# Kernel tuning notes

Measured on AMD Instinct MI355X. Metric: run time of the kernel, lower is better.

The kernel has to match this reference:

```python
import jax, jax.numpy as jnp
import numpy as np

B, T, H, L, V = 32, 512, 1024, 256, 13  # V = FDIM_JOINT_VOCAB_DECODING


def setup_inputs() -> dict:
    key = jax.random.key(0)
    ks = jax.random.split(key, 16)
    s_in = 1.0 / np.sqrt(V)
    s_h = 1.0 / np.sqrt(H)
    s_l = 1.0 / np.sqrt(L)
    s_hl = 1.0 / np.sqrt(H + L)
    # one-hot-like teacher-forced inputs (first token is all-zero start token)
    labels = jax.random.randint(ks[0], (B, T), 0, V)
    seq_input = jax.nn.one_hot(labels, V, dtype=jnp.float32)
    seq_input = jnp.concatenate([jnp.zeros((B, 1, V), jnp.float32), seq_input[:, :-1]], axis=1)
    lengths = jax.random.randint(ks[1], (B,), T // 2, T + 1).astype(jnp.int32)
    return {
        "seq_input": seq_input,
        "latent_vec": jax.random.normal(ks[2], (B, L), jnp.float32),
        "labels": labels.astype(jnp.int32),
        "lengths": lengths,
        "W_ih": jax.random.uniform(ks[3], (4 * H, V), jnp.float32, -s_h, s_h),
        "W_hh": jax.random.uniform(ks[4], (4 * H, H), jnp.float32, -s_h, s_h),
        "b_ih": jax.random.uniform(ks[5], (4 * H,), jnp.float32, -s_h, s_h),
        "b_hh": jax.random.uniform(ks[6], (4 * H,), jnp.float32, -s_h, s_h),
        "Wz": jax.random.uniform(ks[7], (H, L), jnp.float32, -s_l, s_l),
        "bz": jax.random.uniform(ks[8], (H,), jnp.float32, -s_l, s_l),
        "Wnl": jax.random.uniform(ks[9], (H, H + L), jnp.float32, -s_hl, s_hl),
        "bnl": jax.random.uniform(ks[10], (H,), jnp.float32, -s_hl, s_hl),
        "Wout": jax.random.uniform(ks[11], (V, H), jnp.float32, -s_h, s_h),
        "bout": jax.random.uniform(ks[12], (V,), jnp.float32, -s_h, s_h),
    }


def _forward(seq_input, latent_vec, labels, lengths,
             W_ih, W_hh, b_ih, b_hh, Wz, bz, Wnl, bnl, Wout, bout):
    h0 = jax.nn.relu(latent_vec @ Wz.T + bz)              # [B,H]
    c0 = jnp.zeros_like(h0)

    def step(carry, x_t):
        h, c = carry
        gates = x_t @ W_ih.T + b_ih + h @ W_hh.T + b_hh   # [B,4H]
        i, f, g, o = jnp.split(gates, 4, axis=-1)         # torch LSTMCell gate order
        c = jax.nn.sigmoid(f) * c + jax.nn.sigmoid(i) * jnp.tanh(g)
        h = jax.nn.sigmoid(o) * jnp.tanh(c)
        return (h, c), h

    xs = jnp.swapaxes(seq_input, 0, 1)                    # [T,B,V]
    _, hs = jax.lax.scan(step, (h0, c0), xs)              # [T,B,H]
    hs = jnp.swapaxes(hs, 0, 1)                           # [B,T,H]

    # aggregate: cat(h, z) -> relu(W_nonlinear) -> W
    lat = jnp.broadcast_to(latent_vec[:, None, :], (hs.shape[0], hs.shape[1], latent_vec.shape[-1]))
    feat = jnp.concatenate([hs, lat], axis=-1)            # [B,T,H+L]
    logits = jax.nn.relu(feat @ Wnl.T + bnl) @ Wout.T + bout  # [B,T,V]

    logp = jax.nn.log_softmax(logits, axis=-1)
    nll = -jnp.take_along_axis(logp, labels[..., None].astype(jnp.int32), axis=-1)[..., 0]  # [B,T]
    mask = (jnp.arange(T)[None, :] < lengths[:, None]).astype(nll.dtype)
    batch_loss = jnp.sum(nll * mask, axis=1)              # per-sequence segment sum
    return batch_loss


def reference(seq_input, latent_vec, labels, lengths,
              W_ih, W_hh, b_ih, b_hh, Wz, bz, Wnl, bnl, Wout, bout):
    batch_loss = _forward(seq_input, latent_vec, labels, lengths,
                          W_ih, W_hh, b_ih, b_hh, Wz, bz, Wnl, bnl, Wout, bout)
    return jnp.sum(batch_loss), batch_loss
```

## Files before the change

kernel.cpp:

```cpp
#include <hip/hip_runtime.h>
#include <hip/hip_bf16.h>

#define B_   32
#define T_   512
#define H_   1024
#define L_   256
#define V_   13
#define G4H  4096
#define KHL  1280

typedef float f32x4 __attribute__((ext_vector_type(4)));
typedef short s16x8 __attribute__((ext_vector_type(8)));
typedef unsigned short u16;
typedef unsigned int   u32;
typedef unsigned long long u64;

#define OFF_BF   33619968u
#define OFF_BF2  42008576u
#define OFF_AZ   44630016u
#define OFF_BAR  44646400u
#define OFF_MID  44650496u
#define OFF_GX   OFF_MID
#define OFF_TOK  (OFF_MID + 229376u)

__device__ __forceinline__ u16 f2bf(float f) {
    union { float f; u32 u; } v; v.f = f;
    u32 u = v.u;
    u32 r = (u + 0x7fffu + ((u >> 16) & 1u)) >> 16;
    return (u16)r;
}
__device__ __forceinline__ float bf2f(u16 h) {
    union { u32 u; float f; } v; v.u = ((u32)h) << 16;
    return v.f;
}
__device__ __forceinline__ float sigm_(float x) {
    x = fminf(fmaxf(x, -30.f), 30.f);
    return 1.f / (1.f + __expf(-x));
}
__device__ __forceinline__ float tanh_(float x) {
    x = fminf(fmaxf(x, -15.f), 15.f);
    float e = __expf(2.f * x);
    return (e - 1.f) / (e + 1.f);
}

__device__ __forceinline__ u32 afrag_pos(int bl, int k) {
    return (u32)((k >> 5) * 512 + ((bl | (((k >> 3) & 3) << 4)) << 3) + (k & 7));
}

__global__ __launch_bounds__(256) void k_init_misc(
        const float* __restrict__ latent, const float* __restrict__ Wz,
        const float* __restrict__ bz,
        u16* __restrict__ Ax, u16* __restrict__ Az, int* __restrict__ bar) {
    int gid = blockIdx.x * 256 + threadIdx.x;
    int b = gid >> 10, j = gid & 1023;
    const float* lrow = latent + b * L_;
    const float* wrow = Wz + j * L_;
    float acc = bz[j];
    #pragma unroll 4
    for (int l = 0; l < L_; ++l) acc += lrow[l] * wrow[l];
    Ax[(b >> 4) * 16384 + afrag_pos(b & 15, j)] = f2bf(fmaxf(acc, 0.f));
    if (gid < B_ * L_) {
        int bb = gid >> 8, l = gid & 255;
        Az[(bb >> 4) * 4096 + afrag_pos(bb & 15, l)] = f2bf(latent[gid]);
    }
    if (gid < 1024) bar[gid] = 0;
}

__global__ __launch_bounds__(256) void k_init_gx(
        const float* __restrict__ W_ih, const float* __restrict__ b_ih,
        const float* __restrict__ b_hh, float* __restrict__ Gx) {
    int row = blockIdx.x * 256 + threadIdx.x;
    if (row >= G4H) return;
    int gg = row >> 10, jg = row & 1023;
    float base = b_ih[row] + b_hh[row];
    float* d = Gx + (size_t)jg * 56;
    const float* wr = W_ih + (size_t)row * V_;
    #pragma unroll
    for (int t = 0; t < V_; ++t) d[t * 4 + gg] = base + wr[t];
    d[13 * 4 + gg] = base;
}

__global__ __launch_bounds__(256) void k_init_tok(
        const float* __restrict__ seq, u16* __restrict__ tok) {
    int gid = blockIdx.x * 256 + threadIdx.x;
    int s = gid >> 5, b = gid & 31;
    const float* r = seq + ((size_t)b * T_ + s) * V_;
    int t = 13;
    #pragma unroll
    for (int v = 0; v < V_; ++v) if (r[v] > 0.5f) t = v;
    tok[gid] = (u16)t;
}

__global__ __launch_bounds__(256) void k_init_wfrag(
        const float* __restrict__ W_hh, u16* __restrict__ Bf) {
    int base = blockIdx.x * 256 + threadIdx.x;
    #pragma unroll
    for (int i = 0; i < 8; ++i) {
        int idx = base + i * 524288;
        int jv   = idx & 7;
        int lane = (idx >> 3) & 63;
        int kc   = (idx >> 9) & 31;
        int nt   = idx >> 14;
        int u = lane & 15;
        int row = (u & 3) * H_ + nt * 4 + (u >> 2);
        int k = kc * 32 + (lane >> 4) * 8 + jv;
        Bf[idx] = f2bf(W_hh[row * H_ + k]);
    }
}

__global__ __launch_bounds__(256) void k_init_wfrag2(
        const float* __restrict__ Wnl, u16* __restrict__ Bf2) {
    int idx = blockIdx.x * 256 + threadIdx.x;
    for (; idx < 1310720; idx += 524288) {
        int jv   = idx & 7;
        int lane = (idx >> 3) & 63;
        int q    = idx >> 9;
        int kc   = q % 40;
        int nt2  = q / 40;
        int n = nt2 * 16 + (lane & 15);
        int k = kc * 32 + (lane >> 4) * 8 + jv;
        Bf2[idx] = f2bf(Wnl[n * KHL + k]);
    }
}

__global__ __launch_bounds__(512, 1) void k_recur(
        const u16* __restrict__ tokbuf, const float* __restrict__ Gx,
        const u16* __restrict__ Bf, u16* __restrict__ Ax,
        int* __restrict__ bar) {
    __shared__ uint4 AhV[2048];
    int tid = threadIdx.x;
    int bid = blockIdx.x;
    int mt = bid & 1;
    int p  = bid >> 1;
    int w = tid >> 6, L = tid & 63;
    int nt = p * 8 + w;
    int lm = L & 15, quad = L >> 4;

    s16x8 afr[32];
    {
        const u16* bfp = Bf + (size_t)nt * 16384 + L * 8;
        #pragma unroll
        for (int kc = 0; kc < 32; ++kc)
            afr[kc] = *reinterpret_cast<const s16x8*>(bfp + kc * 512);
    }
    int jg = nt * 4 + quad;
    int b = mt * 16 + lm;
    const float* gxp = Gx + (size_t)jg * 56;
    u32 posu16 = (u32)((nt >> 3) * 512 + ((lm | (((nt >> 1) & 3) << 4)) << 3)
                       + (nt & 1) * 4 + quad);
    int* flags = bar + mt * 512;
    const int* myflag = flags + (w + 8 * (L & 3)) * 16;
    u32* AxD = (u32*)Ax;
    float c = 0.f;

    for (int s = 0; s < T_; ++s) {
        int tok = tokbuf[s * 32 + b];
        float4 gx4 = *reinterpret_cast<const float4*>(gxp + tok * 4);

        for (;;) {
            int v = __hip_atomic_load(myflag, __ATOMIC_RELAXED,
                                      __HIP_MEMORY_SCOPE_AGENT);
            if (__all(v >= s)) break;
            __builtin_amdgcn_s_sleep(1);
        }
        const uint4* srcq = (const uint4*)((const char*)Ax
                             + ((size_t)s * 2 + mt) * 32768);
        #pragma unroll
        for (int i = 0; i < 4; ++i)
            AhV[i * 512 + tid] = srcq[i * 512 + tid];
        __syncthreads();

        f32x4 a0 = {0.f,0.f,0.f,0.f}, a1 = {0.f,0.f,0.f,0.f};
        f32x4 a2 = {0.f,0.f,0.f,0.f}, a3 = {0.f,0.f,0.f,0.f};
        const u16* hp = (const u16*)AhV + L * 8;
        #pragma unroll
        for (int kc = 0; kc < 32; kc += 4) {
            s16x8 h0 = *reinterpret_cast<const s16x8*>(hp + kc * 512);
            s16x8 h1 = *reinterpret_cast<const s16x8*>(hp + (kc + 1) * 512);
            s16x8 h2 = *reinterpret_cast<const s16x8*>(hp + (kc + 2) * 512);
            s16x8 h3 = *reinterpret_cast<const s16x8*>(hp + (kc + 3) * 512);
            a0 = __builtin_amdgcn_mfma_f32_16x16x32_bf16(afr[kc],     h0, a0, 0, 0, 0);
            a1 = __builtin_amdgcn_mfma_f32_16x16x32_bf16(afr[kc + 1], h1, a1, 0, 0, 0);
            a2 = __builtin_amdgcn_mfma_f32_16x16x32_bf16(afr[kc + 2], h2, a2, 0, 0, 0);
            a3 = __builtin_amdgcn_mfma_f32_16x16x32_bf16(afr[kc + 3], h3, a3, 0, 0, 0);
        }
        float gi = a0[0] + a1[0] + a2[0] + a3[0] + gx4.x;
        float gf = a0[1] + a1[1] + a2[1] + a3[1] + gx4.y;
        float gg = a0[2] + a1[2] + a2[2] + a3[2] + gx4.z;
        float go = a0[3] + a1[3] + a2[3] + a3[3] + gx4.w;
        float ig = sigm_(gi), fg = sigm_(gf);
        float gt = tanh_(gg), og = sigm_(go);
        c = fg * c + ig * gt;
        float hv = og * tanh_(c);

        u32 bits = (u32)f2bf(hv);
        u32 other = (u32)(u16)__shfl_xor((int)bits, 16);
        if (!(quad & 1)) {
            u32 word = bits | (other << 16);
            __hip_atomic_store(
                AxD + ((size_t)(s + 1) * 2 + mt) * 8192 + (posu16 >> 1),
                word, __ATOMIC_RELAXED, __HIP_MEMORY_SCOPE_AGENT);
        }
        if (s == T_ - 1) break;
        __syncthreads();
        if (tid == 0)
            __hip_atomic_store(flags + p * 16, s + 1, __ATOMIC_RELAXED,
                               __HIP_MEMORY_SCOPE_AGENT);
    }
}

__global__ __launch_bounds__(256) void k_gemm1(
        const u16* __restrict__ Ax, const u16* __restrict__ Az,
        const u16* __restrict__ Bf2, const float* __restrict__ bnl,
        u16* __restrict__ mid) {
    int tid = threadIdx.x;
    int nb = blockIdx.x;
    int mb = blockIdx.y;
    int w = tid >> 6, L = tid & 63;
    int lm = L & 15, quad = L >> 4;
    int mti0 = mb * 8 + w * 2;
    const u16* a0p = Ax + ((size_t)mti0 + 2) * 16384 + L * 8;
    const u16* a1p = a0p + 16384;
    const u16* az0 = Az + L * 8;
    const u16* az1 = az0 + 4096;
    const u16* bp = Bf2 + (size_t)(nb * 4) * 40 * 512 + L * 8;

    f32x4 acc[2][4];
    #pragma unroll
    for (int a = 0; a < 2; ++a)
        #pragma unroll
        for (int n = 0; n < 4; ++n) acc[a][n] = (f32x4){0.f, 0.f, 0.f, 0.f};

    #pragma unroll 4
    for (int kc = 0; kc < 32; ++kc) {
        s16x8 a0 = *reinterpret_cast<const s16x8*>(a0p + kc * 512);
        s16x8 a1 = *reinterpret_cast<const s16x8*>(a1p + kc * 512);
        #pragma unroll
        for (int n4 = 0; n4 < 4; ++n4) {
            s16x8 bv = *reinterpret_cast<const s16x8*>(bp + ((size_t)n4 * 40 + kc) * 512);
            acc[0][n4] = __builtin_amdgcn_mfma_f32_16x16x32_bf16(a0, bv, acc[0][n4], 0, 0, 0);
            acc[1][n4] = __builtin_amdgcn_mfma_f32_16x16x32_bf16(a1, bv, acc[1][n4], 0, 0, 0);
        }
    }
    #pragma unroll
    for (int kc2 = 0; kc2 < 8; ++kc2) {
        s16x8 a0 = *reinterpret_cast<const s16x8*>(az0 + kc2 * 512);
        s16x8 a1 = *reinterpret_cast<const s16x8*>(az1 + kc2 * 512);
        #pragma unroll
        for (int n4 = 0; n4 < 4; ++n4) {
            s16x8 bv = *reinterpret_cast<const s16x8*>(bp + ((size_t)n4 * 40 + 32 + kc2) * 512);
            acc[0][n4] = __builtin_amdgcn_mfma_f32_16x16x32_bf16(a0, bv, acc[0][n4], 0, 0, 0);
            acc[1][n4] = __builtin_amdgcn_mfma_f32_16x16x32_bf16(a1, bv, acc[1][n4], 0, 0, 0);
        }
    }
    #pragma unroll
    for (int mt2 = 0; mt2 < 2; ++mt2)
        #pragma unroll
        for (int n4 = 0; n4 < 4; ++n4)
            #pragma unroll
            for (int r = 0; r < 4; ++r) {
                int m = mb * 128 + w * 32 + mt2 * 16 + quad * 4 + r;
                int n = (nb * 4 + n4) * 16 + lm;
                float v = acc[mt2][n4][r] + bnl[n];
                mid[(size_t)m * H_ + n] = f2bf(fmaxf(v, 0.f));
            }
}

__global__ __launch_bounds__(256) void k_loss(
        const u16* __restrict__ mid, const float* __restrict__ Wout,
        const float* __restrict__ bout, const int* __restrict__ labels,
        const int* __restrict__ lengths, float* __restrict__ out) {
    int mrow = blockIdx.x;
    int b = mrow & 31, t = mrow >> 5;
    if (t >= lengths[b]) return;
    int tid = threadIdx.x;
    float p[V_];
    #pragma unroll
    for (int v = 0; v < V_; ++v) p[v] = 0.f;
    uint2 raw = *reinterpret_cast<const uint2*>(mid + (size_t)mrow * H_ + tid * 4);
    const u16* rs = (const u16*)&raw;
    float mv0 = bf2f(rs[0]), mv1 = bf2f(rs[1]), mv2 = bf2f(rs[2]), mv3 = bf2f(rs[3]);
    #pragma unroll
    for (int v = 0; v < V_; ++v) {
        float4 wv = *reinterpret_cast<const float4*>(Wout + v * H_ + tid * 4);
        p[v] = mv0 * wv.x + mv1 * wv.y + mv2 * wv.z + mv3 * wv.w;
    }
    #pragma unroll
    for (int off = 32; off > 0; off >>= 1)
        #pragma unroll
        for (int v = 0; v < V_; ++v) p[v] += __shfl_down(p[v], off);
    __shared__ float red[4][V_];
    int w = tid >> 6, L = tid & 63;
    if (L == 0)
        #pragma unroll
        for (int v = 0; v < V_; ++v) red[w][v] = p[v];
    __syncthreads();
    if (tid == 0) {
        float lg[V_]; float mx = -1e30f;
        #pragma unroll
        for (int v = 0; v < V_; ++v) {
            lg[v] = red[0][v] + red[1][v] + red[2][v] + red[3][v] + bout[v];
            mx = fmaxf(mx, lg[v]);
        }
        float se = 0.f;
        #pragma unroll
        for (int v = 0; v < V_; ++v) se += __expf(lg[v] - mx);
        float lse = mx + logf(se);
        int lab = labels[b * T_ + t];
        atomicAdd(&out[1 + b], lse - lg[lab]);
    }
}

__global__ void k_final(float* __restrict__ out) {
    float s = 0.f;
    for (int b = 0; b < B_; ++b) s += out[1 + b];
    out[0] = s;
}

extern "C" void kernel_launch(void* const* d_in, const int* in_sizes, int n_in,
                              void* d_out, int out_size, void* d_ws, size_t ws_size,
                              hipStream_t stream) {
    const float* seq    = (const float*)d_in[0];
    const float* latent = (const float*)d_in[1];
    const int*   labels = (const int*)d_in[2];
    const int*   lengths= (const int*)d_in[3];
    const float* W_ih   = (const float*)d_in[4];
    const float* W_hh   = (const float*)d_in[5];
    const float* b_ih   = (const float*)d_in[6];
    const float* b_hh   = (const float*)d_in[7];
    const float* Wz     = (const float*)d_in[8];
    const float* bz     = (const float*)d_in[9];
    const float* Wnl    = (const float*)d_in[10];
    const float* bnl    = (const float*)d_in[11];
    const float* Wout   = (const float*)d_in[12];
    const float* bout   = (const float*)d_in[13];

    char* ws = (char*)d_ws;
    u16*   Ax   = (u16*)(ws);
    u16*   Bf   = (u16*)(ws + OFF_BF);
    u16*   Bf2  = (u16*)(ws + OFF_BF2);
    u16*   Az   = (u16*)(ws + OFF_AZ);
    int*   bar  = (int*)(ws + OFF_BAR);
    u16*   mid  = (u16*)(ws + OFF_MID);
    float* Gx   = (float*)(ws + OFF_GX);
    u16*   tok  = (u16*)(ws + OFF_TOK);
    float* out  = (float*)d_out;

    hipMemsetAsync(d_out, 0, 33 * sizeof(float), stream);
    k_init_misc<<<128, 256, 0, stream>>>(latent, Wz, bz, Ax, Az, bar);
    k_init_gx<<<16, 256, 0, stream>>>(W_ih, b_ih, b_hh, Gx);
    k_init_tok<<<64, 256, 0, stream>>>(seq, tok);
    k_init_wfrag<<<2048, 256, 0, stream>>>(W_hh, Bf);
    k_init_wfrag2<<<2048, 256, 0, stream>>>(Wnl, Bf2);
    k_recur<<<64, 512, 0, stream>>>(tok, Gx, Bf, Ax, bar);
    k_gemm1<<<dim3(16, 128), 256, 0, stream>>>(Ax, Az, Bf2, bnl, mid);
    k_loss<<<16384, 256, 0, stream>>>(mid, Wout, bout, labels, lengths, out);
    k_final<<<1, 1, 0, stream>>>(out);
}
```

Before: 1.409 ms.

## Replace flag barrier with step-tagged data words in a ring buffer

The per-step cross-block flag barrier in the persistent LSTM recurrence is replaced by a 4-slot ring buffer where each hidden-state word carries its step index in the upper 32 bits. Consumers poll the data words directly until every tag matches the current step, then scatter them into a double-buffered LDS tile, which removes the separate flag store, the extra __syncthreads, and the flag-then-data round trip. The cost is more global polling traffic, 64-bit atomic stores with tag overhead, and a ring depth of 4 that relies on the producer never running more than a few steps ahead.

```diff
diff --git a/kernel.cpp b/kernel.cpp
--- a/kernel.cpp
+++ b/kernel.cpp
@@ -22,6 +22,7 @@
 #define OFF_MID  44650496u
 #define OFF_GX   OFF_MID
 #define OFF_TOK  (OFF_MID + 229376u)
+#define OFF_AXT  (OFF_MID + 262144u)
 
 __device__ __forceinline__ u16 f2bf(float f) {
     union { float f; u32 u; } v; v.f = f;
@@ -50,7 +51,8 @@
 __global__ __launch_bounds__(256) void k_init_misc(
         const float* __restrict__ latent, const float* __restrict__ Wz,
         const float* __restrict__ bz,
-        u16* __restrict__ Ax, u16* __restrict__ Az, int* __restrict__ bar) {
+        u16* __restrict__ Ax, u16* __restrict__ Az, int* __restrict__ bar,
+        char* __restrict__ AxT) {
     int gid = blockIdx.x * 256 + threadIdx.x;
     int b = gid >> 10, j = gid & 1023;
     const float* lrow = latent + b * L_;
@@ -58,7 +60,24 @@
     float acc = bz[j];
     #pragma unroll 4
     for (int l = 0; l < L_; ++l) acc += lrow[l] * wrow[l];
-    Ax[(b >> 4) * 16384 + afrag_pos(b & 15, j)] = f2bf(fmaxf(acc, 0.f));
+    float h0 = fmaxf(acc, 0.f);
+    u16 h0b = f2bf(h0);
+    Ax[(b >> 4) * 16384 + afrag_pos(b & 15, j)] = h0b;
+    {
+        int mt = b >> 4, lm = b & 15, nt = j >> 2, q = j & 3;
+        u16* gr = (u16*)(AxT + ((size_t)(mt) * 4096 + nt * 16 + lm) * 16);
+        gr[q < 2 ? q : q + 2] = h0b;
+        if (q == 0) {
+            u32* gd = (u32*)gr;
+            gd[1] = 0u; gd[3] = 0u;
+            #pragma unroll
+            for (int k2 = 1; k2 < 4; ++k2) {
+                u32* gp = (u32*)(AxT + ((size_t)(k2 * 2 + mt) * 4096
+                                        + nt * 16 + lm) * 16);
+                gp[1] = 0xFFFFFFFFu; gp[3] = 0xFFFFFFFFu;
+            }
+        }
+    }
     if (gid < B_ * L_) {
         int bb = gid >> 8, l = gid & 255;
         Az[(bb >> 4) * 4096 + afrag_pos(bb & 15, l)] = f2bf(latent[gid]);
@@ -126,8 +145,8 @@
 __global__ __launch_bounds__(512, 1) void k_recur(
         const u16* __restrict__ tokbuf, const float* __restrict__ Gx,
         const u16* __restrict__ Bf, u16* __restrict__ Ax,
-        int* __restrict__ bar) {
-    __shared__ uint4 AhV[2048];
+        char* __restrict__ AxT) {
+    __shared__ uint4 AhV[2][2048];
     int tid = threadIdx.x;
     int bid = blockIdx.x;
     int mt = bid & 1;
@@ -148,31 +167,54 @@
     const float* gxp = Gx + (size_t)jg * 56;
     u32 posu16 = (u32)((nt >> 3) * 512 + ((lm | (((nt >> 1) & 3) << 4)) << 3)
                        + (nt & 1) * 4 + quad);
-    int* flags = bar + mt * 512;
-    const int* myflag = flags + (w + 8 * (L & 3)) * 16;
     u32* AxD = (u32*)Ax;
     float c = 0.f;
+
+    u32 gbase[8];
+    #pragma unroll
+    for (int i = 0; i < 8; ++i) {
+        int g = tid + i * 512, nt_ = g >> 4, lm_ = g & 15;
+        gbase[i] = (u32)((nt_ >> 3) * 512
+                         + ((lm_ | (((nt_ >> 1) & 3) << 4)) << 3) + (nt_ & 1) * 4);
+    }
 
     for (int s = 0; s < T_; ++s) {
         int tok = tokbuf[s * 32 + b];
         float4 gx4 = *reinterpret_cast<const float4*>(gxp + tok * 4);
 
+        const char* slab = AxT + ((size_t)((s & 3) * 2 + mt)) * 65536;
+        u64 d0[8], d1[8];
+        u32 mask = 0;
         for (;;) {
-            int v = __hip_atomic_load(myflag, __ATOMIC_RELAXED,
-                                      __HIP_MEMORY_SCOPE_AGENT);
-            if (__all(v >= s)) break;
+            #pragma unroll
+            for (int i = 0; i < 8; ++i) {
+                if (!(mask & (1u << i))) {
+                    const u64* gp = (const u64*)(slab
+                                     + ((size_t)(tid + i * 512)) * 16);
+                    d0[i] = __hip_atomic_load(gp, __ATOMIC_RELAXED,
+                                              __HIP_MEMORY_SCOPE_AGENT);
+                    d1[i] = __hip_atomic_load(gp + 1, __ATOMIC_RELAXED,
+                                              __HIP_MEMORY_SCOPE_AGENT);
+                }
+            }
+            #pragma unroll
+            for (int i = 0; i < 8; ++i)
+                if (((u32)(d0[i] >> 32) == (u32)s) &
+                    ((u32)(d1[i] >> 32) == (u32)s))
+                    mask |= (1u << i);
+            if (mask == 0xffu) break;
             __builtin_amdgcn_s_sleep(1);
         }
-        const uint4* srcq = (const uint4*)((const char*)Ax
-                             + ((size_t)s * 2 + mt) * 32768);
-        #pragma unroll
-        for (int i = 0; i < 4; ++i)
-            AhV[i * 512 + tid] = srcq[i * 512 + tid];
+        u16* dst = (u16*)&AhV[s & 1][0];
+        #pragma unroll
+        for (int i = 0; i < 8; ++i)
+            *(u64*)(dst + gbase[i]) =
+                ((u64)(u32)d0[i]) | (((u64)(u32)d1[i]) << 32);
         __syncthreads();
 
         f32x4 a0 = {0.f,0.f,0.f,0.f}, a1 = {0.f,0.f,0.f,0.f};
         f32x4 a2 = {0.f,0.f,0.f,0.f}, a3 = {0.f,0.f,0.f,0.f};
-        const u16* hp = (const u16*)AhV + L * 8;
+        const u16* hp = dst + L * 8;
         #pragma unroll
         for (int kc = 0; kc < 32; kc += 4) {
             s16x8 h0 = *reinterpret_cast<const s16x8*>(hp + kc * 512);
@@ -194,18 +236,24 @@
         float hv = og * tanh_(c);
 
         u32 bits = (u32)f2bf(hv);
-        u32 other = (u32)(u16)__shfl_xor((int)bits, 16);
+        u32 oth = (u32)(u16)__shfl_xor((int)bits, 16);
+        u32 wA = bits | (oth << 16);
+        u32 wB = (u32)__shfl_xor((int)wA, 32);
+
         if (!(quad & 1)) {
-            u32 word = bits | (other << 16);
             __hip_atomic_store(
                 AxD + ((size_t)(s + 1) * 2 + mt) * 8192 + (posu16 >> 1),
-                word, __ATOMIC_RELAXED, __HIP_MEMORY_SCOPE_AGENT);
-        }
-        if (s == T_ - 1) break;
-        __syncthreads();
-        if (tid == 0)
-            __hip_atomic_store(flags + p * 16, s + 1, __ATOMIC_RELAXED,
-                               __HIP_MEMORY_SCOPE_AGENT);
+                wA, __ATOMIC_RELAXED, __HIP_MEMORY_SCOPE_AGENT);
+        }
+        if ((s < T_ - 1) & (L < 16)) {
+            char* gp8 = AxT + ((size_t)(((s + 1) & 3) * 2 + mt)) * 65536
+                        + ((size_t)(nt * 16 + L)) * 16;
+            u64 t = ((u64)(u32)(s + 1)) << 32;
+            __hip_atomic_store((u64*)gp8, (u64)wA | t,
+                               __ATOMIC_RELAXED, __HIP_MEMORY_SCOPE_AGENT);
+            __hip_atomic_store((u64*)gp8 + 1, (u64)wB | t,
+                               __ATOMIC_RELAXED, __HIP_MEMORY_SCOPE_AGENT);
+        }
     }
 }
 
@@ -344,15 +392,16 @@
     u16*   mid  = (u16*)(ws + OFF_MID);
     float* Gx   = (float*)(ws + OFF_GX);
     u16*   tok  = (u16*)(ws + OFF_TOK);
+    char*  AxT  = (char*)(ws + OFF_AXT);
     float* out  = (float*)d_out;
 
     hipMemsetAsync(d_out, 0, 33 * sizeof(float), stream);
-    k_init_misc<<<128, 256, 0, stream>>>(latent, Wz, bz, Ax, Az, bar);
+    k_init_misc<<<128, 256, 0, stream>>>(latent, Wz, bz, Ax, Az, bar, AxT);
     k_init_gx<<<16, 256, 0, stream>>>(W_ih, b_ih, b_hh, Gx);
     k_init_tok<<<64, 256, 0, stream>>>(seq, tok);
     k_init_wfrag<<<2048, 256, 0, stream>>>(W_hh, Bf);
     k_init_wfrag2<<<2048, 256, 0, stream>>>(Wnl, Bf2);
-    k_recur<<<64, 512, 0, stream>>>(tok, Gx, Bf, Ax, bar);
+    k_recur<<<64, 512, 0, stream>>>(tok, Gx, Bf, Ax, AxT);
     k_gemm1<<<dim3(16, 128), 256, 0, stream>>>(Ax, Az, Bf2, bnl, mid);
     k_loss<<<16384, 256, 0, stream>>>(mid, Wout, bout, labels, lengths, out);
     k_final<<<1, 1, 0, stream>>>(out);
```

Measured after the change: 1.787 ms. +26.8%, slower.
